# Performance work log

Hardware: AMD Instinct MI355X
Metric: run time of the kernel (lower is better)

Reference implementation:

```python
import jax, jax.numpy as jnp
import numpy as np

MAT_DIM = 4  # quaternion algebra vector size
EMBED_DIM = 1024
NUM_HEADS = 16
HEAD_DIM = EMBED_DIM // NUM_HEADS  # 64
SCALE = 1.0 / np.sqrt(HEAD_DIM)


def quaternion_structure():
    # C[i,j,k]: e_i * e_j = sum_k C[i,j,k] e_k, basis (1, i, j, k)
    C = np.zeros((4, 4, 4), dtype=np.float32)
    table = [
        (0, 0, 0, 1.0), (0, 1, 1, 1.0), (0, 2, 2, 1.0), (0, 3, 3, 1.0),
        (1, 0, 1, 1.0), (2, 0, 2, 1.0), (3, 0, 3, 1.0),
        (1, 1, 0, -1.0), (2, 2, 0, -1.0), (3, 3, 0, -1.0),
        (1, 2, 3, 1.0), (2, 1, 3, -1.0),
        (2, 3, 1, 1.0), (3, 2, 1, -1.0),
        (3, 1, 2, 1.0), (1, 3, 2, -1.0),
    ]
    for i, j, k, s in table:
        C[i, j, k] = s
    return jnp.asarray(C)


def algebra_linear(x, W, b, C):
    # x: [B,S,Nin,d] algebra-blocked input; W: [Nout,Nin,d]; b: [Nout,d]
    # y[b,s,o,k] = sum_{n,i,j} C[i,j,k] W[o,n,i] x[b,s,n,j] + b[o,k]
    Wm = jnp.einsum('oni,ijk->onjk', W, C)  # left-multiplication matrices
    return jnp.einsum('bsnj,onjk->bsok', x, Wm) + b


def setup_inputs() -> dict:
    key = jax.random.key(0)
    ks = jax.random.split(key, 6)
    B, S = 2, 2048
    nb = EMBED_DIM // MAT_DIM  # 256 algebra blocks
    w_std = 0.02
    inp = {
        'x': jax.random.normal(ks[0], (B, S, EMBED_DIM), dtype=jnp.float32),
        'mask': jnp.ones((1, 1, S, S), dtype=jnp.int32),
        'Wq': jax.random.normal(ks[1], (nb, nb, MAT_DIM), dtype=jnp.float32) * w_std,
        'bq': jnp.zeros((nb, MAT_DIM), dtype=jnp.float32),
        'Wk': jax.random.normal(ks[2], (nb, nb, MAT_DIM), dtype=jnp.float32) * w_std,
        'bk': jnp.zeros((nb, MAT_DIM), dtype=jnp.float32),
        'Wv': jax.random.normal(ks[3], (nb, nb, MAT_DIM), dtype=jnp.float32) * w_std,
        'bv': jnp.zeros((nb, MAT_DIM), dtype=jnp.float32),
        'Wo': jax.random.normal(ks[4], (nb, nb, MAT_DIM), dtype=jnp.float32) * w_std,
        'bo': jnp.zeros((nb, MAT_DIM), dtype=jnp.float32),
    }
    return inp


def reference(x, mask, Wq, bq, Wk, bk, Wv, bv, Wo, bo):
    C = quaternion_structure()
    B, S, E = x.shape
    xb = x.reshape(B, S, E // MAT_DIM, MAT_DIM)

    q = algebra_linear(xb, Wq, bq, C).reshape(B, S, E)
    k = algebra_linear(xb, Wk, bk, C).reshape(B, S, E)
    v = algebra_linear(xb, Wv, bv, C).reshape(B, S, E)

    def split_heads(t):  # [B,S,E] -> [B,H,S,hd]
        return t.reshape(B, S, NUM_HEADS, HEAD_DIM).transpose(0, 2, 1, 3)

    q, k, v = split_heads(q), split_heads(k), split_heads(v)

    scores = jnp.einsum('bhqd,bhkd->bhqk', q, k) * SCALE
    scores = jnp.where(mask == 0, -jnp.inf, scores)
    attn = jax.nn.softmax(scores, axis=-1)
    context = jnp.einsum('bhqk,bhkd->bhqd', attn, v)
    context = context.transpose(0, 2, 1, 3).reshape(B, S, E)

    cb = context.reshape(B, S, E // MAT_DIM, MAT_DIM)
    out = algebra_linear(cb, Wo, bo, C).reshape(B, S, E)
    return out
```

## Files before the change

kernel.cpp:

```cpp
#include <hip/hip_runtime.h>
#include <hip/hip_bf16.h>

typedef __attribute__((ext_vector_type(8))) short bf16x8;
typedef __attribute__((ext_vector_type(4))) float f32x4;
typedef __attribute__((ext_vector_type(8))) float f32x8;
typedef __attribute__((ext_vector_type(16))) float f32x16;
typedef __attribute__((ext_vector_type(4))) unsigned short u16x4;
typedef __attribute__((ext_vector_type(4))) unsigned int u32x4;
typedef __attribute__((ext_vector_type(2))) unsigned int u32x2;

#define LOG2E 1.4426950408889634f
#define SCLOG 0.18033688011118312f
#define EXP2(x) __builtin_amdgcn_exp2f(x)
#define SWZ(r) (((r) & 7) ^ (((r) >> 3) & 3))

static __device__ __forceinline__ unsigned short f2bf(float f) {
  __hip_bfloat16 h = __float2bfloat16(f);
  return __builtin_bit_cast(unsigned short, h);
}
static __device__ __forceinline__ float bf2f(unsigned short u) {
  __hip_bfloat16 h = __builtin_bit_cast(__hip_bfloat16, u);
  return __bfloat162float(h);
}
static __device__ __forceinline__ unsigned cvtpk(float lo, float hg) {
  unsigned r;
  asm("v_cvt_pk_bf16_f32 %0, %1, %2" : "=v"(r) : "v"(lo), "v"(hg));
  return r;
}
static __device__ __forceinline__ bf16x8 ld16(const void* p) {
  return *(const bf16x8*)p;
}
static __device__ __forceinline__ void gload16(const void* g, void* l) {
  __builtin_amdgcn_global_load_lds(
      (const __attribute__((address_space(1))) void*)g,
      (__attribute__((address_space(3))) void*)l, 16, 0, 0);
}

__global__ void prep(const float* __restrict__ x,
                     const int* __restrict__ mask,
                     const float* __restrict__ Wq,
                     const float* __restrict__ Wk,
                     const float* __restrict__ Wv,
                     const float* __restrict__ Wo,
                     unsigned short* __restrict__ xb,
                     unsigned short* __restrict__ Mqkv,
                     unsigned short* __restrict__ Mo,
                     unsigned long long* __restrict__ bits_t)
{
  const int bx = blockIdx.x, tid = threadIdx.x;
  if (bx < 16384) {
    const int g = bx * 256 + tid;
    const unsigned long long w = __ballot(mask[g] != 0);
    if ((tid & 63) == 0) {
      const int idx = g >> 6;
      const int sq = idx >> 5, kw = idx & 31;
      bits_t[(size_t)kw * 2048 + sq] = w;
    }
  } else if (bx < 20480) {
    const int i = (bx - 16384) * 256 + tid;
    const float4 a = ((const float4*)x)[i];
    u32x2 o; o[0] = cvtpk(a.x, a.y); o[1] = cvtpk(a.z, a.w);
    ((u32x2*)xb)[i] = o;
  } else {
    const int e = bx - 20480;
    const int mat = e >> 8;
    const int o = e & 255;
    const int n = tid;
    const float* W = (mat == 0) ? Wq : (mat == 1) ? Wk : (mat == 2) ? Wv : Wo;
    unsigned short* M = (mat < 3) ? (Mqkv + (size_t)mat * 1024 * 1024) : Mo;
    const float4 w = *(const float4*)(W + ((size_t)o * 256 + n) * 4);
    const unsigned short w0 = f2bf(w.x), w1 = f2bf(w.y), w2 = f2bf(w.z), w3 = f2bf(w.w);
#define NG(u) ((unsigned short)((u) ^ 0x8000))
    u16x4 r0; r0[0] = w0;     r0[1] = NG(w1); r0[2] = NG(w2); r0[3] = NG(w3);
    u16x4 r1; r1[0] = w1;     r1[1] = w0;     r1[2] = NG(w3); r1[3] = w2;
    u16x4 r2; r2[0] = w2;     r2[1] = w3;     r2[2] = w0;     r2[3] = NG(w1);
    u16x4 r3; r3[0] = w3;     r3[1] = NG(w2); r3[2] = w1;     r3[3] = w0;
#undef NG
    unsigned short* dst = M + (size_t)(o * 4) * 1024 + n * 4;
    *(u16x4*)(dst)        = r0;
    *(u16x4*)(dst + 1024) = r1;
    *(u16x4*)(dst + 2048) = r2;
    *(u16x4*)(dst + 3072) = r3;
  }
}

template <int MODE, int BM>
__global__ __launch_bounds__(256, 3)
void gemm_bt(const unsigned short* __restrict__ A,
             const unsigned short* __restrict__ Bm,
             const float* __restrict__ bias0,
             const float* __restrict__ bias1,
             const float* __restrict__ bias2,
             unsigned short* __restrict__ out0,
             unsigned short* __restrict__ out1,
             unsigned short* __restrict__ out2,
             float* __restrict__ fout)
{
  constexpr int K = 1024;
  constexpr int FR = BM / 32;
  __shared__ unsigned short As[BM * 64];
  __shared__ unsigned short Bs[128 * 64];
  const int tid = threadIdx.x;
  const int lane = tid & 63;
  const int wave = tid >> 6;
  const int bn = blockIdx.x, bm = blockIdx.y;
  const int wm = wave >> 1, wn = wave & 1;
  const int l15 = lane & 15, l4 = lane >> 4;

  f32x4 zero4 = {0.f, 0.f, 0.f, 0.f};
  f32x4 acc[FR][4];
#pragma unroll
  for (int i = 0; i < FR; ++i)
#pragma unroll
    for (int j = 0; j < 4; ++j) acc[i][j] = zero4;

  for (int kk = 0; kk < K; kk += 64) {
#pragma unroll
    for (int c = 0; c < BM / 32; ++c) {
      const int Lb = (wave * (BM / 32) + c) * 1024;
      const int L = Lb + lane * 16;
      const int row = L >> 7;
      const int slot = (L >> 4) & 7;
      const int ss = slot ^ (row & 7);
      gload16(A + (size_t)(bm * BM + row) * K + kk + ss * 8, (char*)As + Lb);
    }
#pragma unroll
    for (int c = 0; c < 4; ++c) {
      const int Lb = (wave * 4 + c) * 1024;
      const int L = Lb + lane * 16;
      const int row = L >> 7;
      const int slot = (L >> 4) & 7;
      const int ss = slot ^ (row & 7);
      gload16(Bm + (size_t)(bn * 128 + row) * K + kk + ss * 8, (char*)Bs + Lb);
    }
    __syncthreads();
#pragma unroll
    for (int ks = 0; ks < 2; ++ks) {
      bf16x8 af[FR], bfr[4];
#pragma unroll
      for (int i = 0; i < FR; ++i) {
        const int ra = wm * (BM / 2) + i * 16 + l15;
        const int sa = (ks * 4 + l4) ^ (ra & 7);
        af[i] = ld16((const char*)As + ra * 128 + sa * 16);
      }
#pragma unroll
      for (int j = 0; j < 4; ++j) {
        const int rb = wn * 64 + j * 16 + l15;
        const int sb = (ks * 4 + l4) ^ (rb & 7);
        bfr[j] = ld16((const char*)Bs + rb * 128 + sb * 16);
      }
#pragma unroll
      for (int i = 0; i < FR; ++i)
#pragma unroll
        for (int j = 0; j < 4; ++j)
          acc[i][j] = __builtin_amdgcn_mfma_f32_16x16x32_bf16(af[i], bfr[j], acc[i][j], 0, 0, 0);
    }
    __syncthreads();
  }

#pragma unroll
  for (int i = 0; i < FR; ++i) {
    const int t0 = bm * BM + wm * (BM / 2) + i * 16 + l4 * 4;
#pragma unroll
    for (int j = 0; j < 4; ++j) {
      const int e = bn * 128 + wn * 64 + j * 16 + l15;
      f32x4 v = acc[i][j];
      if (MODE == 0) {
        const int which = e >> 10;
        const int e1 = e & 1023;
        const float* bp = (which == 0) ? bias0 : (which == 1 ? bias1 : bias2);
        const float bias = bp[e1];
        if (which == 0) {
#pragma unroll
          for (int r = 0; r < 4; ++r)
            out0[(size_t)(t0 + r) * 1024 + e1] = f2bf((v[r] + bias) * SCLOG);
        } else if (which == 1) {
#pragma unroll
          for (int r = 0; r < 4; ++r)
            out1[(size_t)(t0 + r) * 1024 + e1] = f2bf(v[r] + bias);
        } else {
          const int h = e1 >> 6, d = e1 & 63;
          const int b = t0 >> 11, s = t0 & 2047;
          u16x4 pk;
#pragma unroll
          for (int r = 0; r < 4; ++r) pk[r] = f2bf(v[r] + bias);
          *(u16x4*)&out2[((size_t)((b * 16 + h) * 64 + d)) * 2048 + s] = pk;
        }
      } else {
        const float bias = bias0[e];
#pragma unroll
        for (int r = 0; r < 4; ++r)
          fout[(size_t)(t0 + r) * 1024 + e] = v[r] + bias;
      }
    }
  }
}

__global__ __launch_bounds__(256, 2)
void attn_fwd(const unsigned short* __restrict__ q,
              const unsigned short* __restrict__ k,
              const unsigned short* __restrict__ vt,
              const unsigned long long* __restrict__ mbt,
              unsigned short* __restrict__ po,
              float* __restrict__ sbuf)
{
  constexpr int S = 2048;
  __shared__ __align__(16) unsigned short Ks[2 * 4096];
  __shared__ __align__(16) unsigned short Vs[2 * 4096];

  const int bid = blockIdx.x;
  const int vb = (bid & 7) * 64 + (bid >> 3);
  const int half = vb & 1;
  const int qg = (vb >> 1) & 7;
  const int bh = vb >> 4;
  const int b = bh >> 4, h = bh & 15;

  const int tid = threadIdx.x, lane = tid & 63, wave = tid >> 6;
  const int l31 = lane & 31, hif = lane >> 5;
  const int sq0 = qg * 256 + wave * 64 + l31;
  const int sq1 = sq0 + 32;
  const size_t gq0 = (size_t)b * S + sq0;
  const size_t gq1 = (size_t)b * S + sq1;

  bf16x8 bqfA[4], bqfB[4];
#pragma unroll
  for (int s = 0; s < 4; ++s) {
    bqfA[s] = ld16(q + gq0 * 1024 + h * 64 + s * 16 + hif * 8);
    bqfB[s] = ld16(q + gq1 * 1024 + h * 64 + s * 16 + hif * 8);
  }

  f32x16 o00 = {}, o01 = {}, o10 = {}, o11 = {};
  f32x8 lA8 = {}, lB8 = {};
  const int k0 = half * 16;

#define STAGE(bufi, kti)                                                                  \
  {                                                                                       \
    _Pragma("unroll")                                                                     \
    for (int c = 0; c < 2; ++c) {                                                         \
      const int sl = c * 256 + tid;                                                       \
      const int row = sl >> 3;                                                            \
      const int ss = (sl & 7) ^ SWZ(row);                                                 \
      gload16(k + (size_t)(b * S + (kti) * 64 + row) * 1024 + h * 64 + ss * 8,            \
              (char*)Ks + (bufi) * 8192 + (c * 4 + wave) * 1024);                         \
      gload16(vt + (size_t)(bh * 64 + row) * 2048 + (kti) * 64 + ss * 8,                  \
              (char*)Vs + (bufi) * 8192 + (c * 4 + wave) * 1024);                         \
    }                                                                                     \
  }

  STAGE(0, k0);
  __syncthreads();

  int buf = 0;
  for (int kt = k0; kt < k0 + 16; ++kt) {
    const unsigned long long w0 = mbt[(size_t)kt * 2048 + sq0];
    const unsigned long long w1 = mbt[(size_t)kt * 2048 + sq1];
    if (kt + 1 < k0 + 16) STAGE(buf ^ 1, kt + 1);

    const char* Kb = (const char*)Ks + buf * 8192;
    const char* Vb = (const char*)Vs + buf * 8192;

    const int kr0 = l31, kr1 = 32 + l31;
    bf16x8 ak0[4], ak1[4];
#pragma unroll
    for (int s = 0; s < 4; ++s) {
      ak0[s] = ld16(Kb + kr0 * 128 + (((s * 2 + hif) ^ SWZ(kr0)) << 4));
      ak1[s] = ld16(Kb + kr1 * 128 + (((s * 2 + hif) ^ SWZ(kr1)) << 4));
    }

    f32x16 pA0 = {}, pB0 = {}, pA1 = {}, pB1 = {};
#pragma unroll
    for (int s = 0; s < 4; ++s) {
      pA0 = __builtin_amdgcn_mfma_f32_32x32x16_bf16(ak0[s], bqfA[s], pA0, 0, 0, 0);
      pB0 = __builtin_amdgcn_mfma_f32_32x32x16_bf16(ak0[s], bqfB[s], pB0, 0, 0, 0);
      pA1 = __builtin_amdgcn_mfma_f32_32x32x16_bf16(ak1[s], bqfA[s], pA1, 0, 0, 0);
      pB1 = __builtin_amdgcn_mfma_f32_32x32x16_bf16(ak1[s], bqfB[s], pB1, 0, 0, 0);
    }

    const unsigned wA0 = (unsigned)w0, wA1 = (unsigned)(w0 >> 32);
    const unsigned wB0 = (unsigned)w1, wB1 = (unsigned)(w1 >> 32);
    if (!__all((wA0 & wA1 & wB0 & wB1) == 0xffffffffu)) {
#pragma unroll
      for (int c = 0; c < 16; ++c) {
        const int key = (c & 3) + 8 * (c >> 2) + 4 * hif;
        if (!((wA0 >> key) & 1u)) pA0[c] = -INFINITY;
        if (!((wA1 >> key) & 1u)) pA1[c] = -INFINITY;
        if (!((wB0 >> key) & 1u)) pB0[c] = -INFINITY;
        if (!((wB1 >> key) & 1u)) pB1[c] = -INFINITY;
      }
    }

#pragma unroll
    for (int c = 0; c < 16; ++c) {
      pA0[c] = EXP2(pA0[c]); pA1[c] = EXP2(pA1[c]);
      pB0[c] = EXP2(pB0[c]); pB1[c] = EXP2(pB1[c]);
    }

#pragma unroll
    for (int c = 0; c < 8; ++c) {
      lA8[c] += (pA0[c] + pA0[c + 8]) + (pA1[c] + pA1[c + 8]);
      lB8[c] += (pB0[c] + pB0[c + 8]) + (pB1[c] + pB1[c + 8]);
    }

    u32x4 bpwA[4], bpwB[4];
#pragma unroll
    for (int sub = 0; sub < 2; ++sub) {
      const f32x16 psA = sub ? pA1 : pA0;
      const f32x16 psB = sub ? pB1 : pB0;
#pragma unroll
      for (int ks = 0; ks < 2; ++ks) {
        const int rb2 = ks * 8;
        const int fi = sub * 2 + ks;
        unsigned XA0 = cvtpk(psA[rb2 + 0], psA[rb2 + 1]);
        unsigned XA1 = cvtpk(psA[rb2 + 2], psA[rb2 + 3]);
        unsigned YA0 = cvtpk(psA[rb2 + 4], psA[rb2 + 5]);
        unsigned YA1 = cvtpk(psA[rb2 + 6], psA[rb2 + 7]);
        asm("v_permlane32_swap_b32 %0, %1" : "+v"(XA0), "+v"(YA0));
        asm("v_permlane32_swap_b32 %0, %1" : "+v"(XA1), "+v"(YA1));
        bpwA[fi][0] = XA0; bpwA[fi][1] = XA1; bpwA[fi][2] = YA0; bpwA[fi][3] = YA1;
        unsigned XB0 = cvtpk(psB[rb2 + 0], psB[rb2 + 1]);
        unsigned XB1 = cvtpk(psB[rb2 + 2], psB[rb2 + 3]);
        unsigned YB0 = cvtpk(psB[rb2 + 4], psB[rb2 + 5]);
        unsigned YB1 = cvtpk(psB[rb2 + 6], psB[rb2 + 7]);
        asm("v_permlane32_swap_b32 %0, %1" : "+v"(XB0), "+v"(YB0));
        asm("v_permlane32_swap_b32 %0, %1" : "+v"(XB1), "+v"(YB1));
        bpwB[fi][0] = XB0; bpwB[fi][1] = XB1; bpwB[fi][2] = YB0; bpwB[fi][3] = YB1;
      }
    }

#pragma unroll
    for (int fi = 0; fi < 4; ++fi) {
      const int slot = fi * 2 + hif;
      const int r0 = l31, r1 = 32 + l31;
      bf16x8 v0 = ld16(Vb + r0 * 128 + ((slot ^ SWZ(r0)) << 4));
      bf16x8 v1 = ld16(Vb + r1 * 128 + ((slot ^ SWZ(r1)) << 4));
      const bf16x8 fA = __builtin_bit_cast(bf16x8, bpwA[fi]);
      const bf16x8 fB = __builtin_bit_cast(bf16x8, bpwB[fi]);
      o00 = __builtin_amdgcn_mfma_f32_32x32x16_bf16(v0, fA, o00, 0, 0, 0);
      o01 = __builtin_amdgcn_mfma_f32_32x32x16_bf16(v1, fA, o01, 0, 0, 0);
      o10 = __builtin_amdgcn_mfma_f32_32x32x16_bf16(v0, fB, o10, 0, 0, 0);
      o11 = __builtin_amdgcn_mfma_f32_32x32x16_bf16(v1, fB, o11, 0, 0, 0);
    }

    __syncthreads();
    buf ^= 1;
  }
#undef STAGE

  float tA[4], tB[4];
#pragma unroll
  for (int c = 0; c < 4; ++c) { tA[c] = lA8[c] + lA8[c + 4]; tB[c] = lB8[c] + lB8[c + 4]; }
  float lA = (tA[0] + tA[1]) + (tA[2] + tA[3]);
  float lB = (tB[0] + tB[1]) + (tB[2] + tB[3]);
  lA += __shfl_xor(lA, 32, 64);
  lB += __shfl_xor(lB, 32, 64);

  const float invA = (lA > 0.f) ? 1.f / lA : 0.f;
  const float invB = (lB > 0.f) ? 1.f / lB : 0.f;
  const float sA = (lA > 0.f) ? __log2f(lA) : -1e30f;
  const float sB = (lB > 0.f) ? __log2f(lB) : -1e30f;
  unsigned short* cpA = po + ((size_t)(half * 32 + bh) * 2048 + sq0) * 64;
  unsigned short* cpB = po + ((size_t)(half * 32 + bh) * 2048 + sq1) * 64;
#pragma unroll
  for (int g = 0; g < 4; ++g) {
    u32x2 a0, a1, b0, b1;
    a0[0] = cvtpk(o00[g * 4 + 0] * invA, o00[g * 4 + 1] * invA);
    a0[1] = cvtpk(o00[g * 4 + 2] * invA, o00[g * 4 + 3] * invA);
    a1[0] = cvtpk(o01[g * 4 + 0] * invA, o01[g * 4 + 1] * invA);
    a1[1] = cvtpk(o01[g * 4 + 2] * invA, o01[g * 4 + 3] * invA);
    b0[0] = cvtpk(o10[g * 4 + 0] * invB, o10[g * 4 + 1] * invB);
    b0[1] = cvtpk(o10[g * 4 + 2] * invB, o10[g * 4 + 3] * invB);
    b1[0] = cvtpk(o11[g * 4 + 0] * invB, o11[g * 4 + 1] * invB);
    b1[1] = cvtpk(o11[g * 4 + 2] * invB, o11[g * 4 + 3] * invB);
    *(u32x2*)(cpA + g * 8 + hif * 4) = a0;
    *(u32x2*)(cpA + 32 + g * 8 + hif * 4) = a1;
    *(u32x2*)(cpB + g * 8 + hif * 4) = b0;
    *(u32x2*)(cpB + 32 + g * 8 + hif * 4) = b1;
  }
  if (hif == 0) {
    sbuf[half * 65536 + bh * 2048 + sq0] = sA;
    sbuf[half * 65536 + bh * 2048 + sq1] = sB;
  }
}

__global__ void merge_halves(const unsigned short* __restrict__ po,
                             const float* __restrict__ sbuf,
                             unsigned short* __restrict__ ctx)
{
  const int t = blockIdx.x * 256 + threadIdx.x;
  const int row = t >> 3;
  const int d0 = (t & 7) * 8;
  const int bh = row >> 11, sq = row & 2047;
  const int b = bh >> 4, h = bh & 15;

  const float s0 = sbuf[row];
  const float s1 = sbuf[65536 + row];
  const bf16x8 a = ld16(po + (size_t)row * 64 + d0);
  const bf16x8 c = ld16(po + 4194304 + (size_t)row * 64 + d0);
  const float smax = fmaxf(s0, s1);
  float w0 = EXP2(s0 - smax), w1 = EXP2(s1 - smax);
  const float winv = 1.f / (w0 + w1);
  w0 *= winv; w1 *= winv;

  float f[8];
#pragma unroll
  for (int j = 0; j < 8; ++j)
    f[j] = w0 * bf2f((unsigned short)a[j]) + w1 * bf2f((unsigned short)c[j]);
  u32x4 r;
  r[0] = cvtpk(f[0], f[1]);
  r[1] = cvtpk(f[2], f[3]);
  r[2] = cvtpk(f[4], f[5]);
  r[3] = cvtpk(f[6], f[7]);
  *(u32x4*)(ctx + ((size_t)b * 2048 + sq) * 1024 + h * 64 + d0) = r;
}

extern "C" void kernel_launch(void* const* d_in, const int* in_sizes, int n_in,
                              void* d_out, int out_size, void* d_ws, size_t ws_size,
                              hipStream_t stream)
{
  const float* x  = (const float*)d_in[0];
  const int* mask = (const int*)d_in[1];
  const float* Wq = (const float*)d_in[2];
  const float* bq = (const float*)d_in[3];
  const float* Wk = (const float*)d_in[4];
  const float* bk = (const float*)d_in[5];
  const float* Wv = (const float*)d_in[6];
  const float* bv = (const float*)d_in[7];
  const float* Wo = (const float*)d_in[8];
  const float* bo = (const float*)d_in[9];

  char* ws = (char*)d_ws;
  unsigned short* Mqkv = (unsigned short*)(ws);
  unsigned short* Mo   = (unsigned short*)(ws + (6ull  << 20));
  unsigned short* xb   = (unsigned short*)(ws + (8ull  << 20));
  unsigned short* ctx  = (unsigned short*)(ws + (8ull  << 20));
  unsigned short* qb_  = (unsigned short*)(ws + (16ull << 20));
  unsigned short* kb_  = (unsigned short*)(ws + (24ull << 20));
  unsigned short* vtb  = (unsigned short*)(ws + (32ull << 20));
  unsigned long long* bits = (unsigned long long*)(ws + (40ull << 20));
  float* sbuf = (float*)(ws + (40ull << 20) + (512ull << 10));
  unsigned short* po = (unsigned short*)d_out;

  prep<<<dim3(21504), 256, 0, stream>>>(x, mask, Wq, Wk, Wv, Wo, xb, Mqkv, Mo, bits);
  gemm_bt<0, 128><<<dim3(24, 32), 256, 0, stream>>>(xb, Mqkv, bq, bk, bv, qb_, kb_, vtb, nullptr);
  attn_fwd<<<dim3(512), 256, 0, stream>>>(qb_, kb_, vtb, bits, po, sbuf);
  merge_halves<<<dim3(2048), 256, 0, stream>>>(po, sbuf, ctx);
  gemm_bt<1, 64><<<dim3(8, 64), 256, 0, stream>>>(ctx, Mo, bo, bo, bo, nullptr, nullptr, nullptr,
                                                  (float*)d_out);
}
```

Measured before the change: 109.1 us.

## Stage two key tiles per sync in attention and remap GEMM blocks per XCD

The attention kernel now keeps four K/V buffers in LDS and loads two key tiles per barrier step. Each outer iteration prefetches the next pair while it processes the current pair, so there are half as many __syncthreads and more loads in flight. Both GEMM launches switch to a 1D grid with an XCD-aware block remap so neighbouring tiles land on the same chiplet and share L2. LDS use in attention doubles to 64KB, which may cut occupancy below the two blocks per CU the launch bounds request.

```diff
diff --git a/kernel.cpp b/kernel.cpp
--- a/kernel.cpp
+++ b/kernel.cpp
@@ -84,7 +84,7 @@
   }
 }
 
-template <int MODE, int BM>
+template <int MODE, int BM, int NBN>
 __global__ __launch_bounds__(256, 3)
 void gemm_bt(const unsigned short* __restrict__ A,
              const unsigned short* __restrict__ Bm,
@@ -103,7 +103,10 @@
   const int tid = threadIdx.x;
   const int lane = tid & 63;
   const int wave = tid >> 6;
-  const int bn = blockIdx.x, bm = blockIdx.y;
+  const int bid = blockIdx.x;
+  const int cpx = gridDim.x >> 3;
+  const int vb = (bid & 7) * cpx + (bid >> 3);
+  const int bm = vb / NBN, bn = vb % NBN;
   const int wm = wave >> 1, wn = wave & 1;
   const int l15 = lane & 15, l4 = lane >> 4;
 
@@ -205,8 +208,8 @@
               float* __restrict__ sbuf)
 {
   constexpr int S = 2048;
-  __shared__ __align__(16) unsigned short Ks[2 * 4096];
-  __shared__ __align__(16) unsigned short Vs[2 * 4096];
+  __shared__ __align__(16) unsigned short Ks[4 * 4096];
+  __shared__ __align__(16) unsigned short Vs[4 * 4096];
 
   const int bid = blockIdx.x;
   const int vb = (bid & 7) * 64 + (bid >> 3);
@@ -248,101 +251,107 @@
   }
 
   STAGE(0, k0);
+  STAGE(1, k0 + 1);
   __syncthreads();
 
-  int buf = 0;
-  for (int kt = k0; kt < k0 + 16; ++kt) {
-    const unsigned long long w0 = mbt[(size_t)kt * 2048 + sq0];
-    const unsigned long long w1 = mbt[(size_t)kt * 2048 + sq1];
-    if (kt + 1 < k0 + 16) STAGE(buf ^ 1, kt + 1);
-
-    const char* Kb = (const char*)Ks + buf * 8192;
-    const char* Vb = (const char*)Vs + buf * 8192;
-
-    const int kr0 = l31, kr1 = 32 + l31;
-    bf16x8 ak0[4], ak1[4];
-#pragma unroll
-    for (int s = 0; s < 4; ++s) {
-      ak0[s] = ld16(Kb + kr0 * 128 + (((s * 2 + hif) ^ SWZ(kr0)) << 4));
-      ak1[s] = ld16(Kb + kr1 * 128 + (((s * 2 + hif) ^ SWZ(kr1)) << 4));
-    }
-
-    f32x16 pA0 = {}, pB0 = {}, pA1 = {}, pB1 = {};
-#pragma unroll
-    for (int s = 0; s < 4; ++s) {
-      pA0 = __builtin_amdgcn_mfma_f32_32x32x16_bf16(ak0[s], bqfA[s], pA0, 0, 0, 0);
-      pB0 = __builtin_amdgcn_mfma_f32_32x32x16_bf16(ak0[s], bqfB[s], pB0, 0, 0, 0);
-      pA1 = __builtin_amdgcn_mfma_f32_32x32x16_bf16(ak1[s], bqfA[s], pA1, 0, 0, 0);
-      pB1 = __builtin_amdgcn_mfma_f32_32x32x16_bf16(ak1[s], bqfB[s], pB1, 0, 0, 0);
-    }
-
-    const unsigned wA0 = (unsigned)w0, wA1 = (unsigned)(w0 >> 32);
-    const unsigned wB0 = (unsigned)w1, wB1 = (unsigned)(w1 >> 32);
-    if (!__all((wA0 & wA1 & wB0 & wB1) == 0xffffffffu)) {
+  for (int ktp = 0; ktp < 8; ++ktp) {
+    const int kt = k0 + ktp * 2;
+    const int base = (ktp & 1) * 2;
+    if (ktp < 7) {
+      STAGE(base ^ 2, kt + 2);
+      STAGE((base ^ 2) + 1, kt + 3);
+    }
+#pragma unroll 1
+    for (int j = 0; j < 2; ++j) {
+      const int ktj = kt + j;
+      const unsigned long long w0 = mbt[(size_t)ktj * 2048 + sq0];
+      const unsigned long long w1 = mbt[(size_t)ktj * 2048 + sq1];
+      const char* Kb = (const char*)Ks + (base + j) * 8192;
+      const char* Vb = (const char*)Vs + (base + j) * 8192;
+
+      const int kr0 = l31, kr1 = 32 + l31;
+      bf16x8 ak0[4], ak1[4];
+#pragma unroll
+      for (int s = 0; s < 4; ++s) {
+        ak0[s] = ld16(Kb + kr0 * 128 + (((s * 2 + hif) ^ SWZ(kr0)) << 4));
+        ak1[s] = ld16(Kb + kr1 * 128 + (((s * 2 + hif) ^ SWZ(kr1)) << 4));
+      }
+
+      f32x16 pA0 = {}, pB0 = {}, pA1 = {}, pB1 = {};
+#pragma unroll
+      for (int s = 0; s < 4; ++s) {
+        pA0 = __builtin_amdgcn_mfma_f32_32x32x16_bf16(ak0[s], bqfA[s], pA0, 0, 0, 0);
+        pB0 = __builtin_amdgcn_mfma_f32_32x32x16_bf16(ak0[s], bqfB[s], pB0, 0, 0, 0);
+        pA1 = __builtin_amdgcn_mfma_f32_32x32x16_bf16(ak1[s], bqfA[s], pA1, 0, 0, 0);
+        pB1 = __builtin_amdgcn_mfma_f32_32x32x16_bf16(ak1[s], bqfB[s], pB1, 0, 0, 0);
+      }
+
+      const unsigned wA0 = (unsigned)w0, wA1 = (unsigned)(w0 >> 32);
+      const unsigned wB0 = (unsigned)w1, wB1 = (unsigned)(w1 >> 32);
+      if (!__all((wA0 & wA1 & wB0 & wB1) == 0xffffffffu)) {
+#pragma unroll
+        for (int c = 0; c < 16; ++c) {
+          const int key = (c & 3) + 8 * (c >> 2) + 4 * hif;
+          if (!((wA0 >> key) & 1u)) pA0[c] = -INFINITY;
+          if (!((wA1 >> key) & 1u)) pA1[c] = -INFINITY;
+          if (!((wB0 >> key) & 1u)) pB0[c] = -INFINITY;
+          if (!((wB1 >> key) & 1u)) pB1[c] = -INFINITY;
+        }
+      }
+
 #pragma unroll
       for (int c = 0; c < 16; ++c) {
-        const int key = (c & 3) + 8 * (c >> 2) + 4 * hif;
-        if (!((wA0 >> key) & 1u)) pA0[c] = -INFINITY;
-        if (!((wA1 >> key) & 1u)) pA1[c] = -INFINITY;
-        if (!((wB0 >> key) & 1u)) pB0[c] = -INFINITY;
-        if (!((wB1 >> key) & 1u)) pB1[c] = -INFINITY;
-      }
-    }
-
-#pragma unroll
-    for (int c = 0; c < 16; ++c) {
-      pA0[c] = EXP2(pA0[c]); pA1[c] = EXP2(pA1[c]);
-      pB0[c] = EXP2(pB0[c]); pB1[c] = EXP2(pB1[c]);
-    }
-
-#pragma unroll
-    for (int c = 0; c < 8; ++c) {
-      lA8[c] += (pA0[c] + pA0[c + 8]) + (pA1[c] + pA1[c + 8]);
-      lB8[c] += (pB0[c] + pB0[c + 8]) + (pB1[c] + pB1[c + 8]);
-    }
-
-    u32x4 bpwA[4], bpwB[4];
-#pragma unroll
-    for (int sub = 0; sub < 2; ++sub) {
-      const f32x16 psA = sub ? pA1 : pA0;
-      const f32x16 psB = sub ? pB1 : pB0;
-#pragma unroll
-      for (int ks = 0; ks < 2; ++ks) {
-        const int rb2 = ks * 8;
-        const int fi = sub * 2 + ks;
-        unsigned XA0 = cvtpk(psA[rb2 + 0], psA[rb2 + 1]);
-        unsigned XA1 = cvtpk(psA[rb2 + 2], psA[rb2 + 3]);
-        unsigned YA0 = cvtpk(psA[rb2 + 4], psA[rb2 + 5]);
-        unsigned YA1 = cvtpk(psA[rb2 + 6], psA[rb2 + 7]);
-        asm("v_permlane32_swap_b32 %0, %1" : "+v"(XA0), "+v"(YA0));
-        asm("v_permlane32_swap_b32 %0, %1" : "+v"(XA1), "+v"(YA1));
-        bpwA[fi][0] = XA0; bpwA[fi][1] = XA1; bpwA[fi][2] = YA0; bpwA[fi][3] = YA1;
-        unsigned XB0 = cvtpk(psB[rb2 + 0], psB[rb2 + 1]);
-        unsigned XB1 = cvtpk(psB[rb2 + 2], psB[rb2 + 3]);
-        unsigned YB0 = cvtpk(psB[rb2 + 4], psB[rb2 + 5]);
-        unsigned YB1 = cvtpk(psB[rb2 + 6], psB[rb2 + 7]);
-        asm("v_permlane32_swap_b32 %0, %1" : "+v"(XB0), "+v"(YB0));
-        asm("v_permlane32_swap_b32 %0, %1" : "+v"(XB1), "+v"(YB1));
-        bpwB[fi][0] = XB0; bpwB[fi][1] = XB1; bpwB[fi][2] = YB0; bpwB[fi][3] = YB1;
-      }
-    }
-
-#pragma unroll
-    for (int fi = 0; fi < 4; ++fi) {
-      const int slot = fi * 2 + hif;
-      const int r0 = l31, r1 = 32 + l31;
-      bf16x8 v0 = ld16(Vb + r0 * 128 + ((slot ^ SWZ(r0)) << 4));
-      bf16x8 v1 = ld16(Vb + r1 * 128 + ((slot ^ SWZ(r1)) << 4));
-      const bf16x8 fA = __builtin_bit_cast(bf16x8, bpwA[fi]);
-      const bf16x8 fB = __builtin_bit_cast(bf16x8, bpwB[fi]);
-      o00 = __builtin_amdgcn_mfma_f32_32x32x16_bf16(v0, fA, o00, 0, 0, 0);
-      o01 = __builtin_amdgcn_mfma_f32_32x32x16_bf16(v1, fA, o01, 0, 0, 0);
-      o10 = __builtin_amdgcn_mfma_f32_32x32x16_bf16(v0, fB, o10, 0, 0, 0);
-      o11 = __builtin_amdgcn_mfma_f32_32x32x16_bf16(v1, fB, o11, 0, 0, 0);
-    }
-
+        pA0[c] = EXP2(pA0[c]); pA1[c] = EXP2(pA1[c]);
+        pB0[c] = EXP2(pB0[c]); pB1[c] = EXP2(pB1[c]);
+      }
+
+#pragma unroll
+      for (int c = 0; c < 8; ++c) {
+        lA8[c] += (pA0[c] + pA0[c + 8]) + (pA1[c] + pA1[c + 8]);
+        lB8[c] += (pB0[c] + pB0[c + 8]) + (pB1[c] + pB1[c + 8]);
+      }
+
+      u32x4 bpwA[4], bpwB[4];
+#pragma unroll
+      for (int sub = 0; sub < 2; ++sub) {
+        const f32x16 psA = sub ? pA1 : pA0;
+        const f32x16 psB = sub ? pB1 : pB0;
+#pragma unroll
+        for (int ks = 0; ks < 2; ++ks) {
+          const int rb2 = ks * 8;
+          const int fi = sub * 2 + ks;
+          unsigned XA0 = cvtpk(psA[rb2 + 0], psA[rb2 + 1]);
+          unsigned XA1 = cvtpk(psA[rb2 + 2], psA[rb2 + 3]);
+          unsigned YA0 = cvtpk(psA[rb2 + 4], psA[rb2 + 5]);
+          unsigned YA1 = cvtpk(psA[rb2 + 6], psA[rb2 + 7]);
+          asm("v_permlane32_swap_b32 %0, %1" : "+v"(XA0), "+v"(YA0));
+          asm("v_permlane32_swap_b32 %0, %1" : "+v"(XA1), "+v"(YA1));
+          bpwA[fi][0] = XA0; bpwA[fi][1] = XA1; bpwA[fi][2] = YA0; bpwA[fi][3] = YA1;
+          unsigned XB0 = cvtpk(psB[rb2 + 0], psB[rb2 + 1]);
+          unsigned XB1 = cvtpk(psB[rb2 + 2], psB[rb2 + 3]);
+          unsigned YB0 = cvtpk(psB[rb2 + 4], psB[rb2 + 5]);
+          unsigned YB1 = cvtpk(psB[rb2 + 6], psB[rb2 + 7]);
+          asm("v_permlane32_swap_b32 %0, %1" : "+v"(XB0), "+v"(YB0));
+          asm("v_permlane32_swap_b32 %0, %1" : "+v"(XB1), "+v"(YB1));
+          bpwB[fi][0] = XB0; bpwB[fi][1] = XB1; bpwB[fi][2] = YB0; bpwB[fi][3] = YB1;
+        }
+      }
+
+#pragma unroll
+      for (int fi = 0; fi < 4; ++fi) {
+        const int slot = fi * 2 + hif;
+        const int r0 = l31, r1 = 32 + l31;
+        bf16x8 v0 = ld16(Vb + r0 * 128 + ((slot ^ SWZ(r0)) << 4));
+        bf16x8 v1 = ld16(Vb + r1 * 128 + ((slot ^ SWZ(r1)) << 4));
+        const bf16x8 fA = __builtin_bit_cast(bf16x8, bpwA[fi]);
+        const bf16x8 fB = __builtin_bit_cast(bf16x8, bpwB[fi]);
+        o00 = __builtin_amdgcn_mfma_f32_32x32x16_bf16(v0, fA, o00, 0, 0, 0);
+        o01 = __builtin_amdgcn_mfma_f32_32x32x16_bf16(v1, fA, o01, 0, 0, 0);
+        o10 = __builtin_amdgcn_mfma_f32_32x32x16_bf16(v0, fB, o10, 0, 0, 0);
+        o11 = __builtin_amdgcn_mfma_f32_32x32x16_bf16(v1, fB, o11, 0, 0, 0);
+      }
+    }
     __syncthreads();
-    buf ^= 1;
   }
 #undef STAGE
 
@@ -441,9 +450,9 @@
   unsigned short* po = (unsigned short*)d_out;
 
   prep<<<dim3(21504), 256, 0, stream>>>(x, mask, Wq, Wk, Wv, Wo, xb, Mqkv, Mo, bits);
-  gemm_bt<0, 128><<<dim3(24, 32), 256, 0, stream>>>(xb, Mqkv, bq, bk, bv, qb_, kb_, vtb, nullptr);
+  gemm_bt<0, 128, 24><<<dim3(768), 256, 0, stream>>>(xb, Mqkv, bq, bk, bv, qb_, kb_, vtb, nullptr);
   attn_fwd<<<dim3(512), 256, 0, stream>>>(qb_, kb_, vtb, bits, po, sbuf);
   merge_halves<<<dim3(2048), 256, 0, stream>>>(po, sbuf, ctx);
-  gemm_bt<1, 64><<<dim3(8, 64), 256, 0, stream>>>(ctx, Mo, bo, bo, bo, nullptr, nullptr, nullptr,
-                                                  (float*)d_out);
-}
+  gemm_bt<1, 64, 8><<<dim3(512), 256, 0, stream>>>(ctx, Mo, bo, bo, bo, nullptr, nullptr, nullptr,
+                                                   (float*)d_out);
+}
```

Result: no change. 110.7 us (+1.5%).

## Fuse split-KV merge into attention via atomic last-arriver flag, remap GEMM blocks

Applied to the files above, without the earlier changes.

Removes the separate merge_halves kernel. Each attention block now bumps a per-(bh,qgroup) counter after writing its partial output and log-sum. The second block to finish reads the other half's partial and merges it directly into ctx, reusing its own packed outputs from registers. Separately, both GEMM launches switch to a 1D grid with an XCD-aware block remap (bid&7 striding) to improve L2 locality. The cost is one atomic, two threadfences and a syncthreads per attention block, plus a flag reset block added to prep.

```diff
diff --git a/kernel.cpp b/kernel.cpp
--- a/kernel.cpp
+++ b/kernel.cpp
@@ -26,6 +26,13 @@
   unsigned r;
   asm("v_cvt_pk_bf16_f32 %0, %1, %2" : "=v"(r) : "v"(lo), "v"(hg));
   return r;
+}
+static __device__ __forceinline__ unsigned mg2(unsigned own, unsigned oth, float wm, float wo) {
+  const float lo = wm * bf2f((unsigned short)(own & 0xffffu)) +
+                   wo * bf2f((unsigned short)(oth & 0xffffu));
+  const float hi = wm * bf2f((unsigned short)(own >> 16)) +
+                   wo * bf2f((unsigned short)(oth >> 16));
+  return cvtpk(lo, hi);
 }
 static __device__ __forceinline__ bf16x8 ld16(const void* p) {
   return *(const bf16x8*)p;
@@ -45,7 +52,8 @@
                      unsigned short* __restrict__ xb,
                      unsigned short* __restrict__ Mqkv,
                      unsigned short* __restrict__ Mo,
-                     unsigned long long* __restrict__ bits_t)
+                     unsigned long long* __restrict__ bits_t,
+                     int* __restrict__ flags)
 {
   const int bx = blockIdx.x, tid = threadIdx.x;
   if (bx < 16384) {
@@ -61,7 +69,7 @@
     const float4 a = ((const float4*)x)[i];
     u32x2 o; o[0] = cvtpk(a.x, a.y); o[1] = cvtpk(a.z, a.w);
     ((u32x2*)xb)[i] = o;
-  } else {
+  } else if (bx < 21504) {
     const int e = bx - 20480;
     const int mat = e >> 8;
     const int o = e & 255;
@@ -81,10 +89,12 @@
     *(u16x4*)(dst + 1024) = r1;
     *(u16x4*)(dst + 2048) = r2;
     *(u16x4*)(dst + 3072) = r3;
-  }
-}
-
-template <int MODE, int BM>
+  } else {
+    flags[tid] = 0;
+  }
+}
+
+template <int MODE, int BM, int NBN>
 __global__ __launch_bounds__(256, 3)
 void gemm_bt(const unsigned short* __restrict__ A,
              const unsigned short* __restrict__ Bm,
@@ -103,7 +113,10 @@
   const int tid = threadIdx.x;
   const int lane = tid & 63;
   const int wave = tid >> 6;
-  const int bn = blockIdx.x, bm = blockIdx.y;
+  const int bid = blockIdx.x;
+  const int cpx = gridDim.x >> 3;
+  const int vb = (bid & 7) * cpx + (bid >> 3);
+  const int bm = vb / NBN, bn = vb % NBN;
   const int wm = wave >> 1, wn = wave & 1;
   const int l15 = lane & 15, l4 = lane >> 4;
 
@@ -202,7 +215,9 @@
               const unsigned short* __restrict__ vt,
               const unsigned long long* __restrict__ mbt,
               unsigned short* __restrict__ po,
-              float* __restrict__ sbuf)
+              float* __restrict__ sbuf,
+              unsigned short* __restrict__ ctx,
+              int* __restrict__ flags)
 {
   constexpr int S = 2048;
   __shared__ __align__(16) unsigned short Ks[2 * 4096];
@@ -360,57 +375,66 @@
   const float sB = (lB > 0.f) ? __log2f(lB) : -1e30f;
   unsigned short* cpA = po + ((size_t)(half * 32 + bh) * 2048 + sq0) * 64;
   unsigned short* cpB = po + ((size_t)(half * 32 + bh) * 2048 + sq1) * 64;
+  u32x2 pkA0[4], pkA1[4], pkB0[4], pkB1[4];
 #pragma unroll
   for (int g = 0; g < 4; ++g) {
-    u32x2 a0, a1, b0, b1;
-    a0[0] = cvtpk(o00[g * 4 + 0] * invA, o00[g * 4 + 1] * invA);
-    a0[1] = cvtpk(o00[g * 4 + 2] * invA, o00[g * 4 + 3] * invA);
-    a1[0] = cvtpk(o01[g * 4 + 0] * invA, o01[g * 4 + 1] * invA);
-    a1[1] = cvtpk(o01[g * 4 + 2] * invA, o01[g * 4 + 3] * invA);
-    b0[0] = cvtpk(o10[g * 4 + 0] * invB, o10[g * 4 + 1] * invB);
-    b0[1] = cvtpk(o10[g * 4 + 2] * invB, o10[g * 4 + 3] * invB);
-    b1[0] = cvtpk(o11[g * 4 + 0] * invB, o11[g * 4 + 1] * invB);
-    b1[1] = cvtpk(o11[g * 4 + 2] * invB, o11[g * 4 + 3] * invB);
-    *(u32x2*)(cpA + g * 8 + hif * 4) = a0;
-    *(u32x2*)(cpA + 32 + g * 8 + hif * 4) = a1;
-    *(u32x2*)(cpB + g * 8 + hif * 4) = b0;
-    *(u32x2*)(cpB + 32 + g * 8 + hif * 4) = b1;
+    pkA0[g][0] = cvtpk(o00[g * 4 + 0] * invA, o00[g * 4 + 1] * invA);
+    pkA0[g][1] = cvtpk(o00[g * 4 + 2] * invA, o00[g * 4 + 3] * invA);
+    pkA1[g][0] = cvtpk(o01[g * 4 + 0] * invA, o01[g * 4 + 1] * invA);
+    pkA1[g][1] = cvtpk(o01[g * 4 + 2] * invA, o01[g * 4 + 3] * invA);
+    pkB0[g][0] = cvtpk(o10[g * 4 + 0] * invB, o10[g * 4 + 1] * invB);
+    pkB0[g][1] = cvtpk(o10[g * 4 + 2] * invB, o10[g * 4 + 3] * invB);
+    pkB1[g][0] = cvtpk(o11[g * 4 + 0] * invB, o11[g * 4 + 1] * invB);
+    pkB1[g][1] = cvtpk(o11[g * 4 + 2] * invB, o11[g * 4 + 3] * invB);
+    *(u32x2*)(cpA + g * 8 + hif * 4) = pkA0[g];
+    *(u32x2*)(cpA + 32 + g * 8 + hif * 4) = pkA1[g];
+    *(u32x2*)(cpB + g * 8 + hif * 4) = pkB0[g];
+    *(u32x2*)(cpB + 32 + g * 8 + hif * 4) = pkB1[g];
   }
   if (hif == 0) {
     sbuf[half * 65536 + bh * 2048 + sq0] = sA;
     sbuf[half * 65536 + bh * 2048 + sq1] = sB;
   }
-}
-
-__global__ void merge_halves(const unsigned short* __restrict__ po,
-                             const float* __restrict__ sbuf,
-                             unsigned short* __restrict__ ctx)
-{
-  const int t = blockIdx.x * 256 + threadIdx.x;
-  const int row = t >> 3;
-  const int d0 = (t & 7) * 8;
-  const int bh = row >> 11, sq = row & 2047;
-  const int b = bh >> 4, h = bh & 15;
-
-  const float s0 = sbuf[row];
-  const float s1 = sbuf[65536 + row];
-  const bf16x8 a = ld16(po + (size_t)row * 64 + d0);
-  const bf16x8 c = ld16(po + 4194304 + (size_t)row * 64 + d0);
-  const float smax = fmaxf(s0, s1);
-  float w0 = EXP2(s0 - smax), w1 = EXP2(s1 - smax);
-  const float winv = 1.f / (w0 + w1);
-  w0 *= winv; w1 *= winv;
-
-  float f[8];
-#pragma unroll
-  for (int j = 0; j < 8; ++j)
-    f[j] = w0 * bf2f((unsigned short)a[j]) + w1 * bf2f((unsigned short)c[j]);
-  u32x4 r;
-  r[0] = cvtpk(f[0], f[1]);
-  r[1] = cvtpk(f[2], f[3]);
-  r[2] = cvtpk(f[4], f[5]);
-  r[3] = cvtpk(f[6], f[7]);
-  *(u32x4*)(ctx + ((size_t)b * 2048 + sq) * 1024 + h * 64 + d0) = r;
+
+  __threadfence();
+  __shared__ int oldflag;
+  if (tid == 0) oldflag = atomicAdd(&flags[bh * 8 + qg], 1);
+  __syncthreads();
+  if (oldflag == 0) return;
+  __threadfence();
+  const int ho = half ^ 1;
+  const float sOA = sbuf[ho * 65536 + bh * 2048 + sq0];
+  const float sOB = sbuf[ho * 65536 + bh * 2048 + sq1];
+  float mxA = fmaxf(sA, sOA);
+  float wmA = EXP2(sA - mxA), woA = EXP2(sOA - mxA);
+  { const float n = 1.f / (wmA + woA); wmA *= n; woA *= n; }
+  float mxB = fmaxf(sB, sOB);
+  float wmB = EXP2(sB - mxB), woB = EXP2(sOB - mxB);
+  { const float n = 1.f / (wmB + woB); wmB *= n; woB *= n; }
+  const unsigned short* opA = po + ((size_t)(ho * 32 + bh) * 2048 + sq0) * 64;
+  const unsigned short* opB = po + ((size_t)(ho * 32 + bh) * 2048 + sq1) * 64;
+  unsigned short* cxA = ctx + gq0 * 1024 + h * 64;
+  unsigned short* cxB = ctx + gq1 * 1024 + h * 64;
+#pragma unroll
+  for (int g = 0; g < 4; ++g) {
+    const u32x2 qA0 = *(const u32x2*)(opA + g * 8 + hif * 4);
+    const u32x2 qA1 = *(const u32x2*)(opA + 32 + g * 8 + hif * 4);
+    const u32x2 qB0 = *(const u32x2*)(opB + g * 8 + hif * 4);
+    const u32x2 qB1 = *(const u32x2*)(opB + 32 + g * 8 + hif * 4);
+    u32x2 rA0, rA1, rB0, rB1;
+    rA0[0] = mg2(pkA0[g][0], qA0[0], wmA, woA);
+    rA0[1] = mg2(pkA0[g][1], qA0[1], wmA, woA);
+    rA1[0] = mg2(pkA1[g][0], qA1[0], wmA, woA);
+    rA1[1] = mg2(pkA1[g][1], qA1[1], wmA, woA);
+    rB0[0] = mg2(pkB0[g][0], qB0[0], wmB, woB);
+    rB0[1] = mg2(pkB0[g][1], qB0[1], wmB, woB);
+    rB1[0] = mg2(pkB1[g][0], qB1[0], wmB, woB);
+    rB1[1] = mg2(pkB1[g][1], qB1[1], wmB, woB);
+    *(u32x2*)(cxA + g * 8 + hif * 4) = rA0;
+    *(u32x2*)(cxA + 32 + g * 8 + hif * 4) = rA1;
+    *(u32x2*)(cxB + g * 8 + hif * 4) = rB0;
+    *(u32x2*)(cxB + 32 + g * 8 + hif * 4) = rB1;
+  }
 }
 
 extern "C" void kernel_launch(void* const* d_in, const int* in_sizes, int n_in,
@@ -438,12 +462,12 @@
   unsigned short* vtb  = (unsigned short*)(ws + (32ull << 20));
   unsigned long long* bits = (unsigned long long*)(ws + (40ull << 20));
   float* sbuf = (float*)(ws + (40ull << 20) + (512ull << 10));
+  int* flags  = (int*)(ws + (41ull << 20));
   unsigned short* po = (unsigned short*)d_out;
 
-  prep<<<dim3(21504), 256, 0, stream>>>(x, mask, Wq, Wk, Wv, Wo, xb, Mqkv, Mo, bits);
-  gemm_bt<0, 128><<<dim3(24, 32), 256, 0, stream>>>(xb, Mqkv, bq, bk, bv, qb_, kb_, vtb, nullptr);
-  attn_fwd<<<dim3(512), 256, 0, stream>>>(qb_, kb_, vtb, bits, po, sbuf);
-  merge_halves<<<dim3(2048), 256, 0, stream>>>(po, sbuf, ctx);
-  gemm_bt<1, 64><<<dim3(8, 64), 256, 0, stream>>>(ctx, Mo, bo, bo, bo, nullptr, nullptr, nullptr,
-                                                  (float*)d_out);
-}
+  prep<<<dim3(21505), 256, 0, stream>>>(x, mask, Wq, Wk, Wv, Wo, xb, Mqkv, Mo, bits, flags);
+  gemm_bt<0, 128, 24><<<dim3(768), 256, 0, stream>>>(xb, Mqkv, bq, bk, bv, qb_, kb_, vtb, nullptr);
+  attn_fwd<<<dim3(512), 256, 0, stream>>>(qb_, kb_, vtb, bits, po, sbuf, ctx, flags);
+  gemm_bt<1, 64, 8><<<dim3(512), 256, 0, stream>>>(ctx, Mo, bo, bo, bo, nullptr, nullptr, nullptr,
+                                                   (float*)d_out);
+}
```

Result: slower. 202.1 us (+85.3%).
